# Performance work log

Measured on AMD Instinct MI355X. Metric: run time of the kernel, lower is better.

## Reference

```python
import jax, jax.numpy as jnp
import numpy as np

N_NODES = 50000
N_EDGES = 600000
DIMS = [1280, 512, 300, 300]


def setup_inputs() -> dict:
    key = jax.random.key(0)
    ks = jax.random.split(key, 8)
    x = jax.random.normal(ks[0], (N_NODES, DIMS[0]), dtype=jnp.float32)
    edge_index = jax.random.randint(ks[1], (2, N_EDGES), 0, N_NODES, dtype=jnp.int64)
    def w(k, i, o):
        return jax.random.normal(k, (i, o), dtype=jnp.float32) * (1.0 / np.sqrt(i))
    W1 = w(ks[2], DIMS[0], DIMS[1]); b1 = jnp.zeros((DIMS[1],), jnp.float32)
    W2 = w(ks[3], DIMS[1], DIMS[2]); b2 = jnp.zeros((DIMS[2],), jnp.float32)
    W3 = w(ks[4], DIMS[2], DIMS[3]); b3 = jnp.zeros((DIMS[3],), jnp.float32)
    return {"x": x, "W1": W1, "b1": b1, "W2": W2, "b2": b2,
            "W3": W3, "b3": b3, "edge_index": edge_index}


def gcn_conv(x, W, b, src, dst, n):
    """PyG GCNConv: add self-loops, symmetric D^-1/2 (A+I) D^-1/2 aggregation."""
    h = x @ W  # [N, out]
    loops = jnp.arange(n, dtype=src.dtype)
    s = jnp.concatenate([src, loops])  # [E+N]
    d = jnp.concatenate([dst, loops])
    deg = jax.ops.segment_sum(jnp.ones_like(d, dtype=h.dtype), d, num_segments=n)
    dinv = jnp.where(deg > 0, jax.lax.rsqrt(deg), 0.0)
    norm = dinv[s] * dinv[d]  # [E+N]
    out = jax.ops.segment_sum(h[s] * norm[:, None], d, num_segments=n)
    return out + b


def reference(x, W1, b1, W2, b2, W3, b3, edge_index):
    src, dst = edge_index[0], edge_index[1]
    n = x.shape[0]
    # dropout is identity in eval mode; pertubed=False path
    h = jax.nn.relu(gcn_conv(x, W1, b1, src, dst, n))
    h = jax.nn.relu(gcn_conv(h, W2, b2, src, dst, n))
    h = jax.nn.relu(gcn_conv(h, W3, b3, src, dst, n))
    return h  # [N, 300]; per-graph split is a trivial mask over data.batch
```

## Files before the change

### kernel.cpp

```cpp
#include <hip/hip_runtime.h>

typedef _Float16 f16;
typedef _Float16 f16x2 __attribute__((ext_vector_type(2)));
typedef _Float16 f16x4 __attribute__((ext_vector_type(4)));
typedef _Float16 f16x8 __attribute__((ext_vector_type(8)));
typedef float f32x4 __attribute__((ext_vector_type(4)));

#define N_NODES 50000
#define N_EDGES 600000

__device__ __forceinline__ void gl_lds16(const void* g, void* l) {
  __builtin_amdgcn_global_load_lds(
      (__attribute__((address_space(1))) void*)(g),
      (__attribute__((address_space(3))) void*)(l), 16, 0, 0);
}

__global__ void k_setup(const float* __restrict__ x, f16* __restrict__ xh,
                        const float* __restrict__ W1, f16* __restrict__ w1h,
                        const float* __restrict__ W2, f16* __restrict__ w2h,
                        const float* __restrict__ W3, f16* __restrict__ w3h,
                        const float* __restrict__ b2, float* __restrict__ bp2,
                        const float* __restrict__ b3, float* __restrict__ bp3,
                        const int* __restrict__ edst, int* __restrict__ deg) {
  const int b = blockIdx.x, t = threadIdx.x;
  if (b < 62500) {
    long i = (long)b * 256 + t;
    float4 v = ((const float4*)x)[i];
    f16x4 o;
    o[0] = (f16)v.x; o[1] = (f16)v.y; o[2] = (f16)v.z; o[3] = (f16)v.w;
    ((f16x4*)xh)[i] = o;
  } else if (b < 64844) {
    int e = (b - 62500) * 256 + t;
    if (e < N_EDGES) atomicAdd(&deg[edst[e]], 1);
  } else if (b < 67404) {
    int idx = (b - 64844) * 256 + t;
    int n = idx / 1280, k = idx - n * 1280;
    w1h[idx] = (f16)W1[(size_t)k * 512 + n];
  } else if (b < 68004) {
    int bb = b - 67404;
    int n = bb >> 1, k = (bb & 1) * 256 + t;
    if (k < 512) w2h[(size_t)n * 512 + k] = (f16)W2[(size_t)k * 300 + n];
  } else if (b < 68604) {
    int bb = b - 68004;
    int n = bb >> 1, k = (bb & 1) * 256 + t;
    if (k < 320) w3h[(size_t)n * 320 + k] = (k < 300) ? (f16)W3[(size_t)k * 300 + n] : (f16)0.f;
  } else if (b < 68606) {
    int i = (b - 68604) * 256 + t;
    if (i < 320) bp2[i] = (i < 300) ? b2[i] : 0.f;
  } else {
    int i = (b - 68606) * 256 + t;
    if (i < 320) bp3[i] = (i < 300) ? b3[i] : 0.f;
  }
}

__device__ __forceinline__ int block_incl_scan256(int v, int t) {
  __shared__ int wsum[4];
  const int lane = t & 63, w = t >> 6;
  int incl = v;
#pragma unroll
  for (int off = 1; off < 64; off <<= 1) {
    int u = __shfl_up(incl, off, 64);
    if (lane >= off) incl += u;
  }
  if (lane == 63) wsum[w] = incl;
  __syncthreads();
  int add = 0;
#pragma unroll
  for (int k = 0; k < 4; ++k)
    if (k < w) add += wsum[k];
  return incl + add;
}

__global__ void k_scan1(const int* __restrict__ deg, float* __restrict__ dinv,
                        int* __restrict__ bsum, int n) {
  __shared__ int ws4[4];
  const int t = threadIdx.x, b = blockIdx.x;
  const int i = b * 256 + t;
  int v = (i < n) ? deg[i] : 0;
  if (i < n) dinv[i] = rsqrtf((float)(v + 1));
  int s = v;
#pragma unroll
  for (int off = 1; off < 64; off <<= 1) s += __shfl_xor(s, off, 64);
  if ((t & 63) == 0) ws4[t >> 6] = s;
  __syncthreads();
  if (t == 0) bsum[b] = ws4[0] + ws4[1] + ws4[2] + ws4[3];
}

__global__ void k_scan2(const int* __restrict__ bsum, int* __restrict__ bpre,
                        int* __restrict__ rowptr, int nb, int n) {
  const int t = threadIdx.x;
  int v = (t < nb) ? bsum[t] : 0;
  int incl = block_incl_scan256(v, t);
  if (t < nb) bpre[t] = incl - v;
  if (t == 255) rowptr[n] = incl;
}

__global__ void k_scan3(const int* __restrict__ deg, const int* __restrict__ bpre,
                        int* __restrict__ rowptr, int* __restrict__ rptr2, int n) {
  const int t = threadIdx.x, b = blockIdx.x;
  const int i = b * 256 + t;
  int v = (i < n) ? deg[i] : 0;
  int incl = block_incl_scan256(v, t);
  int ex = bpre[b] + incl - v;
  if (i < n) { rowptr[i] = ex; rptr2[i] = ex; }
}

__global__ void k_fill(const int* __restrict__ src, const int* __restrict__ dst,
                       int* __restrict__ rptr2, int2* __restrict__ meta,
                       const float* __restrict__ dinv, int E) {
  int e = blockIdx.x * 256 + threadIdx.x;
  if (e < E) {
    int d = dst[e], s = src[e];
    int pos = atomicAdd(&rptr2[d], 1);
    float w = dinv[s] * dinv[d];
    meta[pos] = make_int2(s, __float_as_int(w));
  }
}

__global__ __launch_bounds__(256, 2)
void gemm_f16_tn(const f16* __restrict__ A, const f16* __restrict__ B,
                 f16* __restrict__ C, int M, int N, int K,
                 int lda, int ldb, int ldc) {
  __shared__ __align__(16) f16 As[128 * 32];
  __shared__ __align__(16) f16 Bs[128 * 32];
  const int tid = threadIdx.x;
  const int wave = tid >> 6;
  const int lane = tid & 63;
  const int bm = blockIdx.x, bn = blockIdx.y;

  const int srow = tid >> 2;
  const int sunit = (tid & 3) ^ ((tid >> 3) & 3);
  long ar0 = (long)bm * 128 + srow;      if (ar0 > M - 1) ar0 = M - 1;
  long ar1 = (long)bm * 128 + srow + 64; if (ar1 > M - 1) ar1 = M - 1;
  long br0 = (long)bn * 128 + srow;      if (br0 > N - 1) br0 = N - 1;
  long br1 = (long)bn * 128 + srow + 64; if (br1 > N - 1) br1 = N - 1;
  const char* aSrc0 = (const char*)(A + ar0 * lda) + sunit * 16;
  const char* aSrc1 = (const char*)(A + ar1 * lda) + sunit * 16;
  const char* bSrc0 = (const char*)(B + br0 * ldb) + sunit * 16;
  const char* bSrc1 = (const char*)(B + br1 * ldb) + sunit * 16;
  char* ldsA0 = (char*)As + wave * 1024;
  char* ldsA1 = (char*)As + 4096 + wave * 1024;
  char* ldsB0 = (char*)Bs + wave * 1024;
  char* ldsB1 = (char*)Bs + 4096 + wave * 1024;

  const int r16 = lane & 15;
  const int kq = lane >> 4;
  const int wm = wave & 1, wn = wave >> 1;

  int aoff[4], boff[4];
#pragma unroll
  for (int t = 0; t < 4; ++t) {
    int arow = wm * 64 + t * 16 + r16;
    aoff[t] = arow * 64 + ((kq ^ ((arow >> 1) & 3)) << 4);
    int brow = wn * 64 + t * 16 + r16;
    boff[t] = brow * 64 + ((kq ^ ((brow >> 1) & 3)) << 4);
  }

  f32x4 acc[4][4] = {};

  for (int k0 = 0; k0 < K; k0 += 32) {
    __syncthreads();
    size_t kb = (size_t)k0 * 2;
    gl_lds16(aSrc0 + kb, ldsA0);
    gl_lds16(aSrc1 + kb, ldsA1);
    gl_lds16(bSrc0 + kb, ldsB0);
    gl_lds16(bSrc1 + kb, ldsB1);
    __syncthreads();

    f16x8 af[4], bf[4];
#pragma unroll
    for (int t = 0; t < 4; ++t) {
      af[t] = *(const f16x8*)((const char*)As + aoff[t]);
      bf[t] = *(const f16x8*)((const char*)Bs + boff[t]);
    }
#pragma unroll
    for (int mt = 0; mt < 4; ++mt)
#pragma unroll
      for (int nt = 0; nt < 4; ++nt)
        acc[mt][nt] = __builtin_amdgcn_mfma_f32_16x16x32_f16(af[mt], bf[nt], acc[mt][nt], 0, 0, 0);
  }

  const int crow0 = bm * 128 + wm * 64;
  const int ccol0 = bn * 128 + wn * 64;
#pragma unroll
  for (int mt = 0; mt < 4; ++mt)
#pragma unroll
    for (int nt = 0; nt < 4; ++nt)
#pragma unroll
      for (int r = 0; r < 4; ++r) {
        int row = crow0 + mt * 16 + kq * 4 + r;
        int col = ccol0 + nt * 16 + r16;
        if (row < M && col < ldc)
          C[(size_t)row * ldc + col] = (col < N) ? (f16)acc[mt][nt][r] : (f16)0.f;
      }
}

template <int LDH, int ACT, bool F16OUT, int DOUT>
__global__ __launch_bounds__(256, 8)
void agg_relu3(const f16* __restrict__ h, const int* __restrict__ rowptr,
               const int2* __restrict__ meta, const float* __restrict__ dinv,
               const float* __restrict__ bias, void* __restrict__ outp, int nNodes) {
  const int tid = threadIdx.x;
  const int lane = tid & 63;
  const int node = blockIdx.x * 4 + (tid >> 6);
  if (node >= nNodes) return;
  const int r0 = __builtin_amdgcn_readfirstlane(rowptr[node]);
  const int r1 = __builtin_amdgcn_readfirstlane(rowptr[node + 1]);
  const float dv = __builtin_bit_cast(
      float, __builtin_amdgcn_readfirstlane(__builtin_bit_cast(int, dinv[node])));

  const int hoff = (lane < ACT ? lane : ACT - 1) * 8;
  const f16* hp = h + hoff;

  float acc[8];
  {
    f16x8 v = *(const f16x8*)(hp + (size_t)node * LDH);
    const float w0 = dv * dv;
#pragma unroll
    for (int j = 0; j < 8; ++j) acc[j] = w0 * (float)v[j];
  }

  for (int base = r0; base < r1; base += 64) {
    const int idx = base + lane;
    int2 m = (idx < r1) ? meta[idx] : make_int2(0, 0);
    const int cnt = min(64, r1 - base);
    int j = 0;
    for (; j + 2 <= cnt; j += 2) {
      int s0 = __shfl(m.x, j, 64);
      int s1 = __shfl(m.x, j + 1, 64);
      float w0 = __int_as_float(__shfl(m.y, j, 64));
      float w1 = __int_as_float(__shfl(m.y, j + 1, 64));
      f16x8 v0 = *(const f16x8*)(hp + (size_t)s0 * LDH);
      f16x8 v1 = *(const f16x8*)(hp + (size_t)s1 * LDH);
#pragma unroll
      for (int q = 0; q < 8; ++q) acc[q] = fmaf(w0, (float)v0[q], acc[q]);
#pragma unroll
      for (int q = 0; q < 8; ++q) acc[q] = fmaf(w1, (float)v1[q], acc[q]);
    }
    if (j < cnt) {
      int s0 = __shfl(m.x, j, 64);
      float w0 = __int_as_float(__shfl(m.y, j, 64));
      f16x8 v0 = *(const f16x8*)(hp + (size_t)s0 * LDH);
#pragma unroll
      for (int q = 0; q < 8; ++q) acc[q] = fmaf(w0, (float)v0[q], acc[q]);
    }
  }

  float4 bv0 = *(const float4*)(bias + hoff);
  float4 bv1 = *(const float4*)(bias + hoff + 4);
  float o[8];
  o[0] = fmaxf(acc[0] + bv0.x, 0.f); o[1] = fmaxf(acc[1] + bv0.y, 0.f);
  o[2] = fmaxf(acc[2] + bv0.z, 0.f); o[3] = fmaxf(acc[3] + bv0.w, 0.f);
  o[4] = fmaxf(acc[4] + bv1.x, 0.f); o[5] = fmaxf(acc[5] + bv1.y, 0.f);
  o[6] = fmaxf(acc[6] + bv1.z, 0.f); o[7] = fmaxf(acc[7] + bv1.w, 0.f);

  if constexpr (F16OUT) {
    if (lane < ACT) {
      f16x8 ov;
#pragma unroll
      for (int j = 0; j < 8; ++j) ov[j] = (f16)o[j];
      *(f16x8*)((f16*)outp + (size_t)node * LDH + lane * 8) = ov;
    }
  } else {
    float* orow = (float*)outp + (size_t)node * DOUT + lane * 8;
    if (lane * 8 + 4 <= DOUT)
      *(float4*)(orow) = make_float4(o[0], o[1], o[2], o[3]);
    if (lane * 8 + 8 <= DOUT)
      *(float4*)(orow + 4) = make_float4(o[4], o[5], o[6], o[7]);
  }
}

extern "C" void kernel_launch(void* const* d_in, const int* in_sizes, int n_in,
                              void* d_out, int out_size, void* d_ws, size_t ws_size,
                              hipStream_t stream) {
  const float* x  = (const float*)d_in[0];
  const float* W1 = (const float*)d_in[1];
  const float* b1 = (const float*)d_in[2];
  const float* W2 = (const float*)d_in[3];
  const float* b2 = (const float*)d_in[4];
  const float* W3 = (const float*)d_in[5];
  const float* b3 = (const float*)d_in[6];
  const int* eidx = (const int*)d_in[7];
  const int* esrc = eidx;
  const int* edst = eidx + N_EDGES;
  float* out = (float*)d_out;

  char* ws = (char*)d_ws;
  f16* xh = (f16*)(ws);
  f16* h2 = (f16*)(ws);
  f16* g2 = (f16*)(ws + 32000000);
  f16* h3 = (f16*)(ws + 64000000);
  f16* h1 = (f16*)(ws + 128000000);
  f16* g1 = (f16*)(ws + 179200000);
  f16* w1h = (f16*)(ws + 230400000);
  f16* w2h = (f16*)(ws + 231710720);
  f16* w3h = (f16*)(ws + 232017920);
  float* bp2 = (float*)(ws + 232209920);
  float* bp3 = (float*)(ws + 232211200);
  int* deg    = (int*)(ws + 232212480);
  float* dinv = (float*)(ws + 232412480);
  int* rowptr = (int*)(ws + 232612480);
  int* rptr2  = (int*)(ws + 232812484);
  int* bsum   = (int*)(ws + 233012488);
  int* bpre   = (int*)(ws + 233013288);
  int2* meta  = (int2*)(ws + 233014088);

  hipMemsetAsync(deg, 0, N_NODES * sizeof(int), stream);

  k_setup<<<68608, 256, 0, stream>>>(x, xh, W1, w1h, W2, w2h, W3, w3h,
                                     b2, bp2, b3, bp3, edst, deg);

  k_scan1<<<196, 256, 0, stream>>>(deg, dinv, bsum, N_NODES);
  k_scan2<<<1, 256, 0, stream>>>(bsum, bpre, rowptr, 196, N_NODES);
  k_scan3<<<196, 256, 0, stream>>>(deg, bpre, rowptr, rptr2, N_NODES);
  k_fill<<<2344, 256, 0, stream>>>(esrc, edst, rptr2, meta, dinv, N_EDGES);

  gemm_f16_tn<<<dim3(391, 4), 256, 0, stream>>>(xh, w1h, h1, N_NODES, 512, 1280, 1280, 1280, 512);
  agg_relu3<512, 64, true, 0><<<12500, 256, 0, stream>>>(h1, rowptr, meta, dinv, b1, g1, N_NODES);

  gemm_f16_tn<<<dim3(391, 3), 256, 0, stream>>>(g1, w2h, h2, N_NODES, 300, 512, 512, 512, 320);
  agg_relu3<320, 40, true, 0><<<12500, 256, 0, stream>>>(h2, rowptr, meta, dinv, bp2, g2, N_NODES);

  gemm_f16_tn<<<dim3(391, 3), 256, 0, stream>>>(g2, w3h, h3, N_NODES, 300, 320, 320, 320, 320);
  agg_relu3<320, 38, false, 300><<<12500, 256, 0, stream>>>(h3, rowptr, meta, dinv, bp3, out, N_NODES);
}
```

Baseline: 817.6 us.

## Double-buffer GEMM LDS tiles and swap grid order for A-tile reuse

The f16 GEMM now keeps two LDS buffers and issues the next K-slice's global-to-LDS loads before computing on the current slice, with one barrier per iteration instead of two. The grid axes are swapped so consecutive blocks share the same row tile of A, which should improve L2 reuse. Launch bounds are raised to target three blocks per CU. LDS use doubles, and correctness relies on the load wait being placed before the barrier.

```diff
diff --git a/kernel.cpp b/kernel.cpp
--- a/kernel.cpp
+++ b/kernel.cpp
@@ -117,16 +117,16 @@
   }
 }
 
-__global__ __launch_bounds__(256, 2)
+__global__ __launch_bounds__(256, 3)
 void gemm_f16_tn(const f16* __restrict__ A, const f16* __restrict__ B,
                  f16* __restrict__ C, int M, int N, int K,
                  int lda, int ldb, int ldc) {
-  __shared__ __align__(16) f16 As[128 * 32];
-  __shared__ __align__(16) f16 Bs[128 * 32];
+  __shared__ __align__(16) f16 As[2][128 * 32];
+  __shared__ __align__(16) f16 Bs[2][128 * 32];
   const int tid = threadIdx.x;
   const int wave = tid >> 6;
   const int lane = tid & 63;
-  const int bm = blockIdx.x, bn = blockIdx.y;
+  const int bm = blockIdx.y, bn = blockIdx.x;
 
   const int srow = tid >> 2;
   const int sunit = (tid & 3) ^ ((tid >> 3) & 3);
@@ -138,10 +138,6 @@
   const char* aSrc1 = (const char*)(A + ar1 * lda) + sunit * 16;
   const char* bSrc0 = (const char*)(B + br0 * ldb) + sunit * 16;
   const char* bSrc1 = (const char*)(B + br1 * ldb) + sunit * 16;
-  char* ldsA0 = (char*)As + wave * 1024;
-  char* ldsA1 = (char*)As + 4096 + wave * 1024;
-  char* ldsB0 = (char*)Bs + wave * 1024;
-  char* ldsB1 = (char*)Bs + 4096 + wave * 1024;
 
   const int r16 = lane & 15;
   const int kq = lane >> 4;
@@ -158,26 +154,39 @@
 
   f32x4 acc[4][4] = {};
 
+  gl_lds16(aSrc0, (char*)As + wave * 1024);
+  gl_lds16(aSrc1, (char*)As + 4096 + wave * 1024);
+  gl_lds16(bSrc0, (char*)Bs + wave * 1024);
+  gl_lds16(bSrc1, (char*)Bs + 4096 + wave * 1024);
+  __syncthreads();
+
+  int buf = 0;
   for (int k0 = 0; k0 < K; k0 += 32) {
-    __syncthreads();
-    size_t kb = (size_t)k0 * 2;
-    gl_lds16(aSrc0 + kb, ldsA0);
-    gl_lds16(aSrc1 + kb, ldsA1);
-    gl_lds16(bSrc0 + kb, ldsB0);
-    gl_lds16(bSrc1 + kb, ldsB1);
-    __syncthreads();
-
+    if (k0 + 32 < K) {
+      const size_t kb = (size_t)(k0 + 32) * 2;
+      const int nb = buf ^ 1;
+      gl_lds16(aSrc0 + kb, (char*)As + nb * 8192 + wave * 1024);
+      gl_lds16(aSrc1 + kb, (char*)As + nb * 8192 + 4096 + wave * 1024);
+      gl_lds16(bSrc0 + kb, (char*)Bs + nb * 8192 + wave * 1024);
+      gl_lds16(bSrc1 + kb, (char*)Bs + nb * 8192 + 4096 + wave * 1024);
+    }
+
+    const char* baseA = (const char*)As + buf * 8192;
+    const char* baseB = (const char*)Bs + buf * 8192;
     f16x8 af[4], bf[4];
 #pragma unroll
     for (int t = 0; t < 4; ++t) {
-      af[t] = *(const f16x8*)((const char*)As + aoff[t]);
-      bf[t] = *(const f16x8*)((const char*)Bs + boff[t]);
+      af[t] = *(const f16x8*)(baseA + aoff[t]);
+      bf[t] = *(const f16x8*)(baseB + boff[t]);
     }
 #pragma unroll
     for (int mt = 0; mt < 4; ++mt)
 #pragma unroll
       for (int nt = 0; nt < 4; ++nt)
         acc[mt][nt] = __builtin_amdgcn_mfma_f32_16x16x32_f16(af[mt], bf[nt], acc[mt][nt], 0, 0, 0);
+
+    __syncthreads();
+    buf ^= 1;
   }
 
   const int crow0 = bm * 128 + wm * 64;
@@ -315,12 +324,12 @@
   k_scan3<<<196, 256, 0, stream>>>(deg, bpre, rowptr, rptr2, N_NODES);
   k_fill<<<2344, 256, 0, stream>>>(esrc, edst, rptr2, meta, dinv, N_EDGES);
 
-  gemm_f16_tn<<<dim3(391, 4), 256, 0, stream>>>(xh, w1h, h1, N_NODES, 512, 1280, 1280, 1280, 512);
+  gemm_f16_tn<<<dim3(4, 391), 256, 0, stream>>>(xh, w1h, h1, N_NODES, 512, 1280, 1280, 1280, 512);
   agg_relu3<512, 64, true, 0><<<12500, 256, 0, stream>>>(h1, rowptr, meta, dinv, b1, g1, N_NODES);
 
-  gemm_f16_tn<<<dim3(391, 3), 256, 0, stream>>>(g1, w2h, h2, N_NODES, 300, 512, 512, 512, 320);
+  gemm_f16_tn<<<dim3(3, 391), 256, 0, stream>>>(g1, w2h, h2, N_NODES, 300, 512, 512, 512, 320);
   agg_relu3<320, 40, true, 0><<<12500, 256, 0, stream>>>(h2, rowptr, meta, dinv, bp2, g2, N_NODES);
 
-  gemm_f16_tn<<<dim3(391, 3), 256, 0, stream>>>(g2, w3h, h3, N_NODES, 300, 320, 320, 320, 320);
+  gemm_f16_tn<<<dim3(3, 391), 256, 0, stream>>>(g2, w3h, h3, N_NODES, 300, 320, 320, 320, 320);
   agg_relu3<320, 38, false, 300><<<12500, 256, 0, stream>>>(h3, rowptr, meta, dinv, bp3, out, N_NODES);
 }
```

Measured after the change: 815.3 us. No clear change (-0.3%).
